# Optimization experiments

Measured on AMD Instinct MI355X. Metric: run time of the kernel, lower is better.

The kernel has to match this reference:

```python
import jax, jax.numpy as jnp
import numpy as np

N_NODES = 100000   # total atoms in the batched graph
N_EDGES = 1600000  # bonds (directed), avg degree 16
N_GRAPHS = 2000    # molecules in the batch
D_IN, D_H, D_OUT = 600, 300, 2  # 600 = embedding_dim(150) * 4


def setup_inputs() -> dict:
    key = jax.random.key(0)
    ks = jax.random.split(key, 8)
    node_feats = jax.random.normal(ks[0], (N_NODES, D_IN), dtype=jnp.float32)
    W1 = jax.random.normal(ks[1], (D_IN, D_H), dtype=jnp.float32) * (1.0 / np.sqrt(D_IN))
    b1 = jnp.zeros((D_H,), dtype=jnp.float32)
    W2 = jax.random.normal(ks[2], (D_H, D_H), dtype=jnp.float32) * (1.0 / np.sqrt(D_H))
    b2 = jnp.zeros((D_H,), dtype=jnp.float32)
    Wfc = jax.random.normal(ks[3], (D_H, D_OUT), dtype=jnp.float32) * (1.0 / np.sqrt(D_H))
    bfc = jnp.zeros((D_OUT,), dtype=jnp.float32)
    src = jax.random.randint(ks[4], (N_EDGES,), 0, N_NODES, dtype=jnp.int32).astype(jnp.int64)
    dst = jax.random.randint(ks[5], (N_EDGES,), 0, N_NODES, dtype=jnp.int32).astype(jnp.int64)
    graph_id = jnp.sort(jax.random.randint(ks[6], (N_NODES,), 0, N_GRAPHS, dtype=jnp.int32)).astype(jnp.int64)
    return {"node_feats": node_feats, "W1": W1, "b1": b1, "W2": W2, "b2": b2,
            "Wfc": Wfc, "bfc": bfc, "src": src, "dst": dst, "graph_id": graph_id}


def _gcn_layer(x, W, b, src, dst, inv_sqrt_out, inv_sqrt_in):
    # DGL GraphConv (norm='both'): h_i = d_i^{-1/2} * sum_{j->i} d_j^{-1/2} (x_j W) + b
    # weight applied before aggregation (in_feats >= out_feats path), math identical either way.
    h = x @ W                                  # [N, d_out]
    m = h * inv_sqrt_out[:, None]              # scale by src out-degree^{-1/2}
    agg = jax.ops.segment_sum(m[src], dst, num_segments=N_NODES)  # [N, d_out]
    return agg * inv_sqrt_in[:, None] + b


def reference(node_feats, W1, b1, W2, b2, Wfc, bfc, src, dst, graph_id):
    ones_e = jnp.ones((src.shape[0],), dtype=node_feats.dtype)
    deg_out = jax.ops.segment_sum(ones_e, src, num_segments=N_NODES)
    deg_in = jax.ops.segment_sum(ones_e, dst, num_segments=N_NODES)
    inv_sqrt_out = jnp.where(deg_out > 0, jax.lax.rsqrt(jnp.maximum(deg_out, 1.0)), 0.0)
    inv_sqrt_in = jnp.where(deg_in > 0, jax.lax.rsqrt(jnp.maximum(deg_in, 1.0)), 0.0)

    h = jax.nn.relu(_gcn_layer(node_feats, W1, b1, src, dst, inv_sqrt_out, inv_sqrt_in))
    h = jax.nn.relu(_gcn_layer(h, W2, b2, src, dst, inv_sqrt_out, inv_sqrt_in))
    p = jax.nn.softmax(h @ Wfc + bfc, axis=-1)  # [N, 2] per-node class probs

    # per-graph mean pooling (unbatch + mean over each graph's nodes)
    pooled_sum = jax.ops.segment_sum(p, graph_id, num_segments=N_GRAPHS)
    counts = jax.ops.segment_sum(jnp.ones((N_NODES,), dtype=p.dtype), graph_id, num_segments=N_GRAPHS)
    return pooled_sum / jnp.maximum(counts, 1.0)[:, None]  # [G, 2]
```

## Files before the change

### kernel.cpp

```cpp
#include <hip/hip_runtime.h>
#include <hip/hip_bf16.h>
#include <hip/hip_fp8.h>

#define N_NODES 100000
#define N_EDGES 1600000
#define N_GRAPHS 2000
#define D_IN 600
#define D_H 300
#define D_OUT 2

#define NPAD 320
#define K1PAD 640
#define K2PAD 320
#define MPAD 100096

typedef __bf16 bf16;
typedef __bf16 bf16x8 __attribute__((ext_vector_type(8)));
typedef float f32x4 __attribute__((ext_vector_type(4)));
typedef float f32x2 __attribute__((ext_vector_type(2)));

__device__ __forceinline__ unsigned char ff8(float f) {
    __hip_fp8_e4m3 t(f); return (unsigned char)t.__x;
}

__global__ __launch_bounds__(256) void count_deg(const int* __restrict__ src,
                                                 const int* __restrict__ dst,
                                                 int* __restrict__ deg_out,
                                                 int* __restrict__ deg_in) {
    int e = blockIdx.x * blockDim.x + threadIdx.x;
    if (e < N_EDGES) {
        atomicAdd(&deg_out[src[e]], 1);
        atomicAdd(&deg_in[dst[e]], 1);
    }
}

__global__ __launch_bounds__(256) void block_sum(const int* __restrict__ deg_in,
                                                 int* __restrict__ bsum) {
    __shared__ int s[256];
    int i = blockIdx.x * 256 + threadIdx.x;
    s[threadIdx.x] = (i < N_NODES) ? deg_in[i] : 0;
    __syncthreads();
    for (int off = 128; off; off >>= 1) {
        if (threadIdx.x < off) s[threadIdx.x] += s[threadIdx.x + off];
        __syncthreads();
    }
    if (threadIdx.x == 0) bsum[blockIdx.x] = s[0];
}

__global__ void scan_serial(const int* __restrict__ bsum, int* __restrict__ boff, int nb) {
    if (threadIdx.x == 0 && blockIdx.x == 0) {
        int run = 0;
        for (int i = 0; i < nb; ++i) { boff[i] = run; run += bsum[i]; }
    }
}

__global__ __launch_bounds__(256) void node_offsets(const int* __restrict__ deg_in,
                                                    const int* __restrict__ deg_out,
                                                    const int* __restrict__ boff,
                                                    int* __restrict__ row_start,
                                                    int* __restrict__ cursor,
                                                    float* __restrict__ inv_in,
                                                    float* __restrict__ inv_out) {
    __shared__ int s[256];
    int i = blockIdx.x * 256 + threadIdx.x;
    int d = (i < N_NODES) ? deg_in[i] : 0;
    s[threadIdx.x] = d;
    __syncthreads();
    for (int off = 1; off < 256; off <<= 1) {
        int v = 0;
        if (threadIdx.x >= off) v = s[threadIdx.x - off];
        __syncthreads();
        if (threadIdx.x >= off) s[threadIdx.x] += v;
        __syncthreads();
    }
    if (i < N_NODES) {
        int excl = s[threadIdx.x] - d;
        int rs = boff[blockIdx.x] + excl;
        row_start[i] = rs;
        cursor[i] = rs;
        int di = deg_in[i];
        int dout = deg_out[i];
        inv_in[i]  = (di   > 0) ? rsqrtf((float)di)   : 0.0f;
        inv_out[i] = (dout > 0) ? rsqrtf((float)dout) : 0.0f;
    }
}

__global__ __launch_bounds__(256) void fill_csr(const int* __restrict__ src,
                                                const int* __restrict__ dst,
                                                int* __restrict__ cursor,
                                                int* __restrict__ adj) {
    int e = blockIdx.x * blockDim.x + threadIdx.x;
    if (e < N_EDGES) {
        int pos = atomicAdd(&cursor[dst[e]], 1);
        adj[pos] = src[e];
    }
}

__global__ __launch_bounds__(256) void conv_bt(const float* __restrict__ W, bf16* __restrict__ Bt,
                                               int K, int N, int Kpad) {
    int idx = blockIdx.x * 256 + threadIdx.x;
    int k = idx % Kpad;
    int n = idx / Kpad;
    if (n >= NPAD) return;
    bf16 v = (bf16)0.0f;
    if (k < K && n < N) v = (bf16)W[(size_t)k * N + n];
    Bt[(size_t)n * Kpad + k] = v;
}

__global__ __launch_bounds__(256) void prep_small(const float* __restrict__ b1,
                                                  const float* __restrict__ b2,
                                                  const float* __restrict__ Wfc,
                                                  float* __restrict__ b1p,
                                                  float* __restrict__ b2p,
                                                  float* __restrict__ wfcp) {
    int i = blockIdx.x * 256 + threadIdx.x;
    if (i < NPAD) {
        b1p[i] = (i < D_H) ? b1[i] : 0.f;
        b2p[i] = (i < D_H) ? b2[i] : 0.f;
    }
    if (i < NPAD * 2) {
        wfcp[i] = (i < D_H * 2) ? Wfc[i] : 0.f;
    }
}

template<int NK, bool AF32>
__global__ __launch_bounds__(256) void gemm_rs(const float* __restrict__ Af,
                                               const bf16* __restrict__ Ab,
                                               const bf16* __restrict__ Bt,
                                               const float* __restrict__ rowscale,
                                               unsigned char* __restrict__ C8,
                                               int M) {
    __shared__ bf16 As[128 * 64];
    __shared__ bf16 Bs[160 * 64];
    const int tid = threadIdx.x;
    const int lane = tid & 63;
    const int wid = tid >> 6;
    const int wr = wid >> 1;
    const int wc = wid & 1;
    const int blockRow = blockIdx.x * 128;
    const int blockCol = blockIdx.y * 160;
    const int Kpad = NK * 64;
    const size_t rowBytes = (size_t)Kpad * 2;

    f32x4 acc[4][5] = {};

    int aO[4], aRow[4], aKs[4];
    #pragma unroll
    for (int c = 0; c < 4; ++c) {
        int o = c * 4096 + tid * 16;
        int row = o >> 7;
        int slot = (o >> 4) & 7;
        aO[c] = o; aRow[c] = row; aKs[c] = (slot ^ (row & 7)) * 8;
    }
    int bO[5], bRow[5], bKs[5];
    #pragma unroll
    for (int c = 0; c < 5; ++c) {
        int o = c * 4096 + tid * 16;
        int row = o >> 7;
        int slot = (o >> 4) & 7;
        bO[c] = o; bRow[c] = row; bKs[c] = (slot ^ (row & 7)) * 8;
    }

    float4 fA[4][2];
    bf16x8 sA[4];
    bf16x8 sB[5];

    auto loadTile = [&](int t) {
        #pragma unroll
        for (int c = 0; c < 4; ++c) {
            if (AF32) {
                int gr = blockRow + aRow[c];
                int k = t * 64 + aKs[c];
                if (gr < N_NODES && k < D_IN) {
                    const float* p = Af + (size_t)gr * D_IN + k;
                    fA[c][0] = *(const float4*)p;
                    fA[c][1] = *(const float4*)(p + 4);
                } else {
                    fA[c][0] = make_float4(0.f, 0.f, 0.f, 0.f);
                    fA[c][1] = make_float4(0.f, 0.f, 0.f, 0.f);
                }
            } else {
                const char* g = (const char*)Ab + (size_t)(blockRow + aRow[c]) * rowBytes
                                + (size_t)t * 128 + aKs[c] * 2;
                sA[c] = *(const bf16x8*)g;
            }
        }
        #pragma unroll
        for (int c = 0; c < 5; ++c) {
            const char* g = (const char*)Bt + (size_t)(blockCol + bRow[c]) * rowBytes
                            + (size_t)t * 128 + bKs[c] * 2;
            sB[c] = *(const bf16x8*)g;
        }
    };

    loadTile(0);

    for (int t = 0; t < NK; ++t) {
        __syncthreads();
        #pragma unroll
        for (int c = 0; c < 4; ++c) {
            bf16x8 v;
            if (AF32) {
                v[0] = (bf16)fA[c][0].x; v[1] = (bf16)fA[c][0].y;
                v[2] = (bf16)fA[c][0].z; v[3] = (bf16)fA[c][0].w;
                v[4] = (bf16)fA[c][1].x; v[5] = (bf16)fA[c][1].y;
                v[6] = (bf16)fA[c][1].z; v[7] = (bf16)fA[c][1].w;
            } else {
                v = sA[c];
            }
            *(bf16x8*)((char*)As + aO[c]) = v;
        }
        #pragma unroll
        for (int c = 0; c < 5; ++c)
            *(bf16x8*)((char*)Bs + bO[c]) = sB[c];
        __syncthreads();
        if (t + 1 < NK) loadTile(t + 1);
        #pragma unroll
        for (int kk = 0; kk < 2; ++kk) {
            int slot = kk * 4 + (lane >> 4);
            bf16x8 af[4], bfr[5];
            #pragma unroll
            for (int mi = 0; mi < 4; ++mi) {
                int row = wr * 64 + mi * 16 + (lane & 15);
                int addr = row * 128 + ((slot ^ (row & 7)) << 4);
                af[mi] = *(const bf16x8*)((const char*)As + addr);
            }
            #pragma unroll
            for (int ni = 0; ni < 5; ++ni) {
                int row = wc * 80 + ni * 16 + (lane & 15);
                int addr = row * 128 + ((slot ^ (row & 7)) << 4);
                bfr[ni] = *(const bf16x8*)((const char*)Bs + addr);
            }
            #pragma unroll
            for (int mi = 0; mi < 4; ++mi)
                #pragma unroll
                for (int ni = 0; ni < 5; ++ni)
                    acc[mi][ni] = __builtin_amdgcn_mfma_f32_16x16x32_bf16(af[mi], bfr[ni], acc[mi][ni], 0, 0, 0);
        }
    }
    {
        const int qs = lane >> 4;
        const int qo = lane >> 4;
        const int io = (lane >> 2) & 3;
        const int cgo = lane & 3;
        #pragma unroll
        for (int mi = 0; mi < 4; ++mi) {
            int rbase = blockRow + wr * 64 + mi * 16;
            float4 s4 = *(const float4*)(rowscale + rbase + qs * 4);
            int gr = rbase + qo * 4 + io;
            #pragma unroll
            for (int ni = 0; ni < 5; ++ni) {
                unsigned int D = (unsigned int)ff8(acc[mi][ni][0] * s4.x)
                               | ((unsigned int)ff8(acc[mi][ni][1] * s4.y) << 8)
                               | ((unsigned int)ff8(acc[mi][ni][2] * s4.z) << 16)
                               | ((unsigned int)ff8(acc[mi][ni][3] * s4.w) << 24);
                int sbase = (lane & 48) + (cgo << 2);
                unsigned int S0 = (unsigned int)__shfl((int)D, sbase + 0);
                unsigned int S1 = (unsigned int)__shfl((int)D, sbase + 1);
                unsigned int S2 = (unsigned int)__shfl((int)D, sbase + 2);
                unsigned int S3 = (unsigned int)__shfl((int)D, sbase + 3);
                int sh = io * 8;
                unsigned int out = ((S0 >> sh) & 0xffu)
                                 | (((S1 >> sh) & 0xffu) << 8)
                                 | (((S2 >> sh) & 0xffu) << 16)
                                 | (((S3 >> sh) & 0xffu) << 24);
                if (gr < M) {
                    int gc = blockCol + wc * 80 + ni * 16 + (cgo << 2);
                    *(unsigned int*)(C8 + (size_t)gr * NPAD + gc) = out;
                }
            }
        }
    }
}

__device__ __forceinline__ void gather_fp8(const unsigned char* __restrict__ m8,
                                           const int* __restrict__ adj,
                                           int s, int d, int lane, float acc[5]) {
    const int cb = lane * 4;
    const int c4 = 256 + lane;
    int e = 0;
    for (; e + 8 <= d; e += 8) {
        unsigned int u[8], b[8];
        #pragma unroll
        for (int j = 0; j < 8; ++j) {
            const unsigned char* r = m8 + (size_t)adj[s + e + j] * NPAD;
            u[j] = *(const unsigned int*)(r + cb);
            b[j] = r[c4];
        }
        #pragma unroll
        for (int j = 0; j < 8; ++j) {
            f32x2 lo = __builtin_amdgcn_cvt_pk_f32_fp8(u[j], false);
            f32x2 hi = __builtin_amdgcn_cvt_pk_f32_fp8(u[j], true);
            acc[0] += lo[0]; acc[1] += lo[1]; acc[2] += hi[0]; acc[3] += hi[1];
            acc[4] += __builtin_amdgcn_cvt_f32_fp8(b[j], 0);
        }
    }
    if (e + 4 <= d) {
        unsigned int u[4], b[4];
        #pragma unroll
        for (int j = 0; j < 4; ++j) {
            const unsigned char* r = m8 + (size_t)adj[s + e + j] * NPAD;
            u[j] = *(const unsigned int*)(r + cb);
            b[j] = r[c4];
        }
        #pragma unroll
        for (int j = 0; j < 4; ++j) {
            f32x2 lo = __builtin_amdgcn_cvt_pk_f32_fp8(u[j], false);
            f32x2 hi = __builtin_amdgcn_cvt_pk_f32_fp8(u[j], true);
            acc[0] += lo[0]; acc[1] += lo[1]; acc[2] += hi[0]; acc[3] += hi[1];
            acc[4] += __builtin_amdgcn_cvt_f32_fp8(b[j], 0);
        }
        e += 4;
    }
    for (; e < d; ++e) {
        const unsigned char* r = m8 + (size_t)adj[s + e] * NPAD;
        unsigned int u = *(const unsigned int*)(r + cb);
        unsigned int b = r[c4];
        f32x2 lo = __builtin_amdgcn_cvt_pk_f32_fp8(u, false);
        f32x2 hi = __builtin_amdgcn_cvt_pk_f32_fp8(u, true);
        acc[0] += lo[0]; acc[1] += lo[1]; acc[2] += hi[0]; acc[3] += hi[1];
        acc[4] += __builtin_amdgcn_cvt_f32_fp8(b, 0);
    }
}

__global__ __launch_bounds__(256) void aggregate_fp8(const unsigned char* __restrict__ m8,
                                                     const int* __restrict__ row_start,
                                                     const int* __restrict__ deg_in,
                                                     const int* __restrict__ adj,
                                                     const float* __restrict__ inv_in,
                                                     const float* __restrict__ biasp,
                                                     bf16* __restrict__ h) {
    int node = (int)((blockIdx.x * (size_t)blockDim.x + threadIdx.x) >> 6);
    int lane = threadIdx.x & 63;
    if (node >= N_NODES) return;
    int s = row_start[node];
    int d = deg_in[node];
    float acc[5] = {};
    gather_fp8(m8, adj, s, d, lane, acc);
    float sc = inv_in[node];
    int cA = lane * 4;
    int c4 = 256 + lane;
    float4 bq = *(const float4*)(biasp + cA);
    bf16* out = h + (size_t)node * NPAD;
    __bf16 o4[4];
    o4[0] = (bf16)fmaxf(acc[0] * sc + bq.x, 0.f);
    o4[1] = (bf16)fmaxf(acc[1] * sc + bq.y, 0.f);
    o4[2] = (bf16)fmaxf(acc[2] * sc + bq.z, 0.f);
    o4[3] = (bf16)fmaxf(acc[3] * sc + bq.w, 0.f);
    *(float2*)(out + cA) = *(float2*)o4;
    out[c4] = (bf16)fmaxf(acc[4] * sc + biasp[c4], 0.f);
}

__global__ __launch_bounds__(256) void agg2_fc_pool(const unsigned char* __restrict__ m8,
                                                    const int* __restrict__ row_start,
                                                    const int* __restrict__ deg_in,
                                                    const int* __restrict__ adj,
                                                    const float* __restrict__ inv_in,
                                                    const float* __restrict__ biasp,
                                                    const float* __restrict__ wfcp,
                                                    const float* __restrict__ bfc,
                                                    const int* __restrict__ gid,
                                                    float* __restrict__ pooled,
                                                    int* __restrict__ gcount) {
    int node = (int)((blockIdx.x * (size_t)blockDim.x + threadIdx.x) >> 6);
    int lane = threadIdx.x & 63;
    if (node >= N_NODES) return;
    int s = row_start[node];
    int d = deg_in[node];
    float acc[5] = {};
    gather_fp8(m8, adj, s, d, lane, acc);
    float sc = inv_in[node];
    int cA = lane * 4;
    int c4 = 256 + lane;
    float4 bq = *(const float4*)(biasp + cA);
    float h0 = fmaxf(acc[0] * sc + bq.x, 0.f);
    float h1 = fmaxf(acc[1] * sc + bq.y, 0.f);
    float h2 = fmaxf(acc[2] * sc + bq.z, 0.f);
    float h3 = fmaxf(acc[3] * sc + bq.w, 0.f);
    float h4 = fmaxf(acc[4] * sc + biasp[c4], 0.f);
    float4 wA0 = *(const float4*)(wfcp + cA * 2);
    float4 wA1 = *(const float4*)(wfcp + cA * 2 + 4);
    float z0 = h0 * wA0.x + h1 * wA0.z + h2 * wA1.x + h3 * wA1.z;
    float z1 = h0 * wA0.y + h1 * wA0.w + h2 * wA1.y + h3 * wA1.w;
    z0 += h4 * wfcp[c4 * 2];
    z1 += h4 * wfcp[c4 * 2 + 1];
    for (int off = 32; off; off >>= 1) {
        z0 += __shfl_down(z0, off);
        z1 += __shfl_down(z1, off);
    }
    if (lane == 0) {
        float s0 = z0 + bfc[0], s1 = z1 + bfc[1];
        float mx = fmaxf(s0, s1);
        float e0 = __expf(s0 - mx), e1 = __expf(s1 - mx);
        float inv = 1.f / (e0 + e1);
        int g = gid[node];
        atomicAdd(&pooled[g * 2 + 0], e0 * inv);
        atomicAdd(&pooled[g * 2 + 1], e1 * inv);
        atomicAdd(&gcount[g], 1);
    }
}

__global__ __launch_bounds__(256) void finalize(const float* __restrict__ pooled,
                                                const int* __restrict__ gcount,
                                                float* __restrict__ out) {
    int i = blockIdx.x * blockDim.x + threadIdx.x;
    if (i < N_GRAPHS * 2) {
        int g = i >> 1;
        float c = (float)max(gcount[g], 1);
        out[i] = pooled[i] / c;
    }
}

extern "C" void kernel_launch(void* const* d_in, const int* in_sizes, int n_in,
                              void* d_out, int out_size, void* d_ws, size_t ws_size,
                              hipStream_t stream) {
    const float* x   = (const float*)d_in[0];
    const float* W1  = (const float*)d_in[1];
    const float* b1  = (const float*)d_in[2];
    const float* W2  = (const float*)d_in[3];
    const float* b2  = (const float*)d_in[4];
    const float* Wfc = (const float*)d_in[5];
    const float* bfc = (const float*)d_in[6];
    const int* src   = (const int*)d_in[7];
    const int* dst   = (const int*)d_in[8];
    const int* gid   = (const int*)d_in[9];

    char* ws = (char*)d_ws;
    size_t off = 0;
    auto alloc = [&](size_t bytes) -> void* {
        void* p = ws + off;
        off = (off + bytes + 255) & ~(size_t)255;
        return p;
    };
    bf16* h_bf            = (bf16*)alloc((size_t)MPAD * NPAD * 2);
    unsigned char* m8     = (unsigned char*)alloc((size_t)N_NODES * NPAD);
    bf16* B1t    = (bf16*)alloc((size_t)NPAD * K1PAD * 2);
    bf16* B2t    = (bf16*)alloc((size_t)NPAD * K2PAD * 2);
    int*   adj      = (int*)alloc((size_t)N_EDGES * 4);
    int*   row_st   = (int*)alloc((size_t)N_NODES * 4);
    int*   cursor   = (int*)alloc((size_t)N_NODES * 4);
    int*   deg_in   = (int*)alloc((size_t)N_NODES * 4);
    int*   deg_out  = (int*)alloc((size_t)N_NODES * 4);
    float* inv_in   = (float*)alloc((size_t)N_NODES * 4);
    float* inv_out  = (float*)alloc((size_t)N_NODES * 4);
    const int NB = (N_NODES + 255) / 256;
    int*   bsum     = (int*)alloc((size_t)NB * 4);
    int*   boff     = (int*)alloc((size_t)NB * 4);
    float* pooled   = (float*)alloc((size_t)N_GRAPHS * 2 * 4);
    int*   gcount   = (int*)alloc((size_t)N_GRAPHS * 4);
    float* b1p      = (float*)alloc((size_t)NPAD * 4);
    float* b2p      = (float*)alloc((size_t)NPAD * 4);
    float* wfcp     = (float*)alloc((size_t)NPAD * 2 * 4);

    hipMemsetAsync(deg_in, 0, (size_t)N_NODES * 4, stream);
    hipMemsetAsync(deg_out, 0, (size_t)N_NODES * 4, stream);
    hipMemsetAsync(pooled, 0, (size_t)N_GRAPHS * 2 * 4, stream);
    hipMemsetAsync(gcount, 0, (size_t)N_GRAPHS * 4, stream);

    count_deg<<<(N_EDGES + 255) / 256, 256, 0, stream>>>(src, dst, deg_out, deg_in);
    block_sum<<<NB, 256, 0, stream>>>(deg_in, bsum);
    scan_serial<<<1, 64, 0, stream>>>(bsum, boff, NB);
    node_offsets<<<NB, 256, 0, stream>>>(deg_in, deg_out, boff, row_st, cursor, inv_in, inv_out);
    fill_csr<<<(N_EDGES + 255) / 256, 256, 0, stream>>>(src, dst, cursor, adj);

    conv_bt<<<(NPAD * K1PAD + 255) / 256, 256, 0, stream>>>(W1, B1t, D_IN, D_H, K1PAD);
    conv_bt<<<(NPAD * K2PAD + 255) / 256, 256, 0, stream>>>(W2, B2t, D_H, D_H, K2PAD);
    prep_small<<<3, 256, 0, stream>>>(b1, b2, Wfc, b1p, b2p, wfcp);

    dim3 ggrid(MPAD / 128, 2);

    gemm_rs<10, true><<<ggrid, 256, 0, stream>>>(x, nullptr, B1t, inv_out, m8, N_NODES);
    aggregate_fp8<<<(N_NODES * 64 + 255) / 256, 256, 0, stream>>>(m8, row_st, deg_in, adj, inv_in, b1p, h_bf);
    gemm_rs<5, false><<<ggrid, 256, 0, stream>>>(nullptr, h_bf, B2t, inv_out, m8, N_NODES);
    agg2_fc_pool<<<(N_NODES * 64 + 255) / 256, 256, 0, stream>>>(m8, row_st, deg_in, adj, inv_in, b2p,
                                                                 wfcp, bfc, gid, pooled, gcount);
    finalize<<<(N_GRAPHS * 2 + 255) / 256, 256, 0, stream>>>(pooled, gcount, (float*)d_out);
}
```

Measured before the change: 693.3 us.

## Stream GEMM over full-width 32-row tiles reading B from global; parallel block-offset scan

The GEMM tiling changes from 128x160 tiles on a 2D grid to 32-row blocks that cover all 320 output columns. Each block stages its full-K A slab in LDS once and reads B fragments straight from global memory (B is small and L2-resident). This reads the large activation matrix once instead of twice (once per column half) and drops the per-k-tile LDS store/sync pipeline. The cost is more B traffic through the cache, since every block re-reads all of B, and there is no prefetch overlap. Separately, the serial single-thread scan of block sums is replaced by a 512-thread LDS Hillis-Steele scan.

```diff
diff --git a/kernel.cpp b/kernel.cpp
--- a/kernel.cpp
+++ b/kernel.cpp
@@ -47,11 +47,21 @@
     if (threadIdx.x == 0) bsum[blockIdx.x] = s[0];
 }
 
-__global__ void scan_serial(const int* __restrict__ bsum, int* __restrict__ boff, int nb) {
-    if (threadIdx.x == 0 && blockIdx.x == 0) {
-        int run = 0;
-        for (int i = 0; i < nb; ++i) { boff[i] = run; run += bsum[i]; }
-    }
+__global__ __launch_bounds__(512) void scan_lds(const int* __restrict__ bsum,
+                                                int* __restrict__ boff, int nb) {
+    __shared__ int s[512];
+    int tid = threadIdx.x;
+    int v = (tid < nb) ? bsum[tid] : 0;
+    s[tid] = v;
+    __syncthreads();
+    for (int off = 1; off < 512; off <<= 1) {
+        int t = 0;
+        if (tid >= off) t = s[tid - off];
+        __syncthreads();
+        if (tid >= off) s[tid] += t;
+        __syncthreads();
+    }
+    if (tid < nb) boff[tid] = s[tid] - v;
 }
 
 __global__ __launch_bounds__(256) void node_offsets(const int* __restrict__ deg_in,
@@ -124,130 +134,78 @@
 }
 
 template<int NK, bool AF32>
-__global__ __launch_bounds__(256) void gemm_rs(const float* __restrict__ Af,
-                                               const bf16* __restrict__ Ab,
-                                               const bf16* __restrict__ Bt,
-                                               const float* __restrict__ rowscale,
-                                               unsigned char* __restrict__ C8,
-                                               int M) {
-    __shared__ bf16 As[128 * 64];
-    __shared__ bf16 Bs[160 * 64];
+__global__ __launch_bounds__(256) void gemm_stream(const float* __restrict__ Af,
+                                                   const bf16* __restrict__ Ab,
+                                                   const bf16* __restrict__ Bt,
+                                                   const float* __restrict__ rowscale,
+                                                   unsigned char* __restrict__ C8,
+                                                   int M) {
+    __shared__ bf16 As[32 * NK * 64];
     const int tid = threadIdx.x;
     const int lane = tid & 63;
-    const int wid = tid >> 6;
-    const int wr = wid >> 1;
-    const int wc = wid & 1;
-    const int blockRow = blockIdx.x * 128;
-    const int blockCol = blockIdx.y * 160;
+    const int wc = tid >> 6;
+    const int blockRow = blockIdx.x * 32;
     const int Kpad = NK * 64;
-    const size_t rowBytes = (size_t)Kpad * 2;
-
-    f32x4 acc[4][5] = {};
-
-    int aO[4], aRow[4], aKs[4];
+
     #pragma unroll
-    for (int c = 0; c < 4; ++c) {
+    for (int c = 0; c < NK; ++c) {
         int o = c * 4096 + tid * 16;
-        int row = o >> 7;
+        int row = (o >> 7) & 31;
         int slot = (o >> 4) & 7;
-        aO[c] = o; aRow[c] = row; aKs[c] = (slot ^ (row & 7)) * 8;
-    }
-    int bO[5], bRow[5], bKs[5];
-    #pragma unroll
-    for (int c = 0; c < 5; ++c) {
-        int o = c * 4096 + tid * 16;
-        int row = o >> 7;
-        int slot = (o >> 4) & 7;
-        bO[c] = o; bRow[c] = row; bKs[c] = (slot ^ (row & 7)) * 8;
-    }
-
-    float4 fA[4][2];
-    bf16x8 sA[4];
-    bf16x8 sB[5];
-
-    auto loadTile = [&](int t) {
-        #pragma unroll
-        for (int c = 0; c < 4; ++c) {
-            if (AF32) {
-                int gr = blockRow + aRow[c];
-                int k = t * 64 + aKs[c];
-                if (gr < N_NODES && k < D_IN) {
-                    const float* p = Af + (size_t)gr * D_IN + k;
-                    fA[c][0] = *(const float4*)p;
-                    fA[c][1] = *(const float4*)(p + 4);
-                } else {
-                    fA[c][0] = make_float4(0.f, 0.f, 0.f, 0.f);
-                    fA[c][1] = make_float4(0.f, 0.f, 0.f, 0.f);
-                }
-            } else {
-                const char* g = (const char*)Ab + (size_t)(blockRow + aRow[c]) * rowBytes
-                                + (size_t)t * 128 + aKs[c] * 2;
-                sA[c] = *(const bf16x8*)g;
+        int srck = c * 64 + (slot ^ (row & 7)) * 8;
+        int gr = blockRow + row;
+        bf16x8 v = {};
+        if (AF32) {
+            if (gr < N_NODES && srck < D_IN) {
+                const float* p = Af + (size_t)gr * D_IN + srck;
+                float4 f0 = *(const float4*)p;
+                float4 f1 = *(const float4*)(p + 4);
+                v[0] = (bf16)f0.x; v[1] = (bf16)f0.y; v[2] = (bf16)f0.z; v[3] = (bf16)f0.w;
+                v[4] = (bf16)f1.x; v[5] = (bf16)f1.y; v[6] = (bf16)f1.z; v[7] = (bf16)f1.w;
             }
-        }
-        #pragma unroll
-        for (int c = 0; c < 5; ++c) {
-            const char* g = (const char*)Bt + (size_t)(blockCol + bRow[c]) * rowBytes
-                            + (size_t)t * 128 + bKs[c] * 2;
-            sB[c] = *(const bf16x8*)g;
-        }
-    };
-
-    loadTile(0);
-
+        } else {
+            if (gr < N_NODES) {
+                v = *(const bf16x8*)(Ab + (size_t)gr * Kpad + srck);
+            }
+        }
+        *(bf16x8*)((char*)As + o) = v;
+    }
+    __syncthreads();
+
+    f32x4 acc[2][5] = {};
     for (int t = 0; t < NK; ++t) {
-        __syncthreads();
-        #pragma unroll
-        for (int c = 0; c < 4; ++c) {
-            bf16x8 v;
-            if (AF32) {
-                v[0] = (bf16)fA[c][0].x; v[1] = (bf16)fA[c][0].y;
-                v[2] = (bf16)fA[c][0].z; v[3] = (bf16)fA[c][0].w;
-                v[4] = (bf16)fA[c][1].x; v[5] = (bf16)fA[c][1].y;
-                v[6] = (bf16)fA[c][1].z; v[7] = (bf16)fA[c][1].w;
-            } else {
-                v = sA[c];
-            }
-            *(bf16x8*)((char*)As + aO[c]) = v;
-        }
-        #pragma unroll
-        for (int c = 0; c < 5; ++c)
-            *(bf16x8*)((char*)Bs + bO[c]) = sB[c];
-        __syncthreads();
-        if (t + 1 < NK) loadTile(t + 1);
         #pragma unroll
         for (int kk = 0; kk < 2; ++kk) {
             int slot = kk * 4 + (lane >> 4);
-            bf16x8 af[4], bfr[5];
+            bf16x8 af[2], bfr[5];
             #pragma unroll
-            for (int mi = 0; mi < 4; ++mi) {
-                int row = wr * 64 + mi * 16 + (lane & 15);
-                int addr = row * 128 + ((slot ^ (row & 7)) << 4);
+            for (int mi = 0; mi < 2; ++mi) {
+                int row = mi * 16 + (lane & 15);
+                int addr = t * 4096 + row * 128 + ((slot ^ (row & 7)) << 4);
                 af[mi] = *(const bf16x8*)((const char*)As + addr);
             }
             #pragma unroll
             for (int ni = 0; ni < 5; ++ni) {
-                int row = wc * 80 + ni * 16 + (lane & 15);
-                int addr = row * 128 + ((slot ^ (row & 7)) << 4);
-                bfr[ni] = *(const bf16x8*)((const char*)Bs + addr);
+                int brow = wc * 80 + ni * 16 + (lane & 15);
+                bfr[ni] = *(const bf16x8*)(Bt + (size_t)brow * Kpad + t * 64 + slot * 8);
             }
             #pragma unroll
-            for (int mi = 0; mi < 4; ++mi)
+            for (int mi = 0; mi < 2; ++mi)
                 #pragma unroll
                 for (int ni = 0; ni < 5; ++ni)
                     acc[mi][ni] = __builtin_amdgcn_mfma_f32_16x16x32_bf16(af[mi], bfr[ni], acc[mi][ni], 0, 0, 0);
         }
     }
+
     {
         const int qs = lane >> 4;
-        const int qo = lane >> 4;
         const int io = (lane >> 2) & 3;
         const int cgo = lane & 3;
         #pragma unroll
-        for (int mi = 0; mi < 4; ++mi) {
-            int rbase = blockRow + wr * 64 + mi * 16;
+        for (int mi = 0; mi < 2; ++mi) {
+            int rbase = blockRow + mi * 16;
             float4 s4 = *(const float4*)(rowscale + rbase + qs * 4);
-            int gr = rbase + qo * 4 + io;
+            int gr = rbase + qs * 4 + io;
             #pragma unroll
             for (int ni = 0; ni < 5; ++ni) {
                 unsigned int D = (unsigned int)ff8(acc[mi][ni][0] * s4.x)
@@ -265,7 +223,7 @@
                                  | (((S2 >> sh) & 0xffu) << 16)
                                  | (((S3 >> sh) & 0xffu) << 24);
                 if (gr < M) {
-                    int gc = blockCol + wc * 80 + ni * 16 + (cgo << 2);
+                    int gc = wc * 80 + ni * 16 + (cgo << 2);
                     *(unsigned int*)(C8 + (size_t)gr * NPAD + gc) = out;
                 }
             }
@@ -459,7 +417,7 @@
 
     count_deg<<<(N_EDGES + 255) / 256, 256, 0, stream>>>(src, dst, deg_out, deg_in);
     block_sum<<<NB, 256, 0, stream>>>(deg_in, bsum);
-    scan_serial<<<1, 64, 0, stream>>>(bsum, boff, NB);
+    scan_lds<<<1, 512, 0, stream>>>(bsum, boff, NB);
     node_offsets<<<NB, 256, 0, stream>>>(deg_in, deg_out, boff, row_st, cursor, inv_in, inv_out);
     fill_csr<<<(N_EDGES + 255) / 256, 256, 0, stream>>>(src, dst, cursor, adj);
 
@@ -467,11 +425,9 @@
     conv_bt<<<(NPAD * K2PAD + 255) / 256, 256, 0, stream>>>(W2, B2t, D_H, D_H, K2PAD);
     prep_small<<<3, 256, 0, stream>>>(b1, b2, Wfc, b1p, b2p, wfcp);
 
-    dim3 ggrid(MPAD / 128, 2);
-
-    gemm_rs<10, true><<<ggrid, 256, 0, stream>>>(x, nullptr, B1t, inv_out, m8, N_NODES);
+    gemm_stream<10, true><<<MPAD / 32, 256, 0, stream>>>(x, nullptr, B1t, inv_out, m8, N_NODES);
     aggregate_fp8<<<(N_NODES * 64 + 255) / 256, 256, 0, stream>>>(m8, row_st, deg_in, adj, inv_in, b1p, h_bf);
-    gemm_rs<5, false><<<ggrid, 256, 0, stream>>>(nullptr, h_bf, B2t, inv_out, m8, N_NODES);
+    gemm_stream<5, false><<<MPAD / 32, 256, 0, stream>>>(nullptr, h_bf, B2t, inv_out, m8, N_NODES);
     agg2_fc_pool<<<(N_NODES * 64 + 255) / 256, 256, 0, stream>>>(m8, row_st, deg_in, adj, inv_in, b2p,
                                                                  wfcp, bfc, gid, pooled, gcount);
     finalize<<<(N_GRAPHS * 2 + 255) / 256, 256, 0, stream>>>(pooled, gcount, (float*)d_out);
```

After: 792.9 us. 14.4% more time.
